# Kernel tuning notes

Hardware: AMD Instinct MI355X
Metric: run time of the kernel (lower is better)

## Reference

```python
import jax, jax.numpy as jnp
import numpy as np

N_CLS = 7  # only the first 7 channels contribute to the loss

def setup_inputs() -> dict:
    key = jax.random.key(0)
    k1, k2 = jax.random.split(key)
    pred = jax.random.normal(k1, (256, 16384, 8), dtype=jnp.float32)
    gt = jax.random.normal(k2, (256, 16384, 8), dtype=jnp.float32)
    return {"pred": pred, "gt": gt}

def reference(pred, gt):
    # per-batch loss: sum over objects and first 7 channels of squared error
    diff = pred[..., :N_CLS] - gt[..., :N_CLS]  # [B, N, 7]
    return jnp.sum(diff * diff, axis=(1, 2))    # [B]
```

## Files before the change

kernel.cpp:

```cpp
#include <hip/hip_runtime.h>


#define THREADS 256
#define SPLIT 16
#define F4_PER_BATCH (16384 * 2)
#define F4_PER_BLOCK (F4_PER_BATCH / SPLIT)
#define UNROLL 8

__global__ __launch_bounds__(THREADS) void label_loss_kernel(
    const float4* __restrict__ pred,
    const float4* __restrict__ gt,
    float* __restrict__ out)
{
    const int bx  = blockIdx.x;
    const int b   = bx / SPLIT;
    const int seg = bx % SPLIT;
    const long i0 = (long)b * F4_PER_BATCH + (long)seg * F4_PER_BLOCK
                  + threadIdx.x;

    const float m = (threadIdx.x & 1) ? 0.0f : 1.0f;

    float4 p[UNROLL], g[UNROLL];
    #pragma unroll
    for (int k = 0; k < UNROLL; ++k) p[k] = pred[i0 + k * THREADS];
    #pragma unroll
    for (int k = 0; k < UNROLL; ++k) g[k] = gt[i0 + k * THREADS];

    float acc[UNROLL];
    #pragma unroll
    for (int k = 0; k < UNROLL; ++k) {
        const float dx = p[k].x - g[k].x;
        const float dy = p[k].y - g[k].y;
        const float dz = p[k].z - g[k].z;
        const float dw = p[k].w - g[k].w;
        acc[k] = dx * dx + dy * dy + dz * dz + m * (dw * dw);
    }

    float v = ((acc[0] + acc[1]) + (acc[2] + acc[3]))
            + ((acc[4] + acc[5]) + (acc[6] + acc[7]));

    #pragma unroll
    for (int off = 32; off > 0; off >>= 1)
        v += __shfl_down(v, off, 64);

    __shared__ float wsum[THREADS / 64];
    const int lane = threadIdx.x & 63;
    const int wave = threadIdx.x >> 6;
    if (lane == 0) wsum[wave] = v;
    __syncthreads();

    if (threadIdx.x == 0) {
        atomicAdd(&out[b], wsum[0] + wsum[1] + wsum[2] + wsum[3]);
    }
}

extern "C" void kernel_launch(void* const* d_in, const int* in_sizes, int n_in,
                              void* d_out, int out_size, void* d_ws, size_t ws_size,
                              hipStream_t stream) {
    const float4* pred = (const float4*)d_in[0];
    const float4* gt   = (const float4*)d_in[1];
    float* out = (float*)d_out;

    hipMemsetAsync(d_out, 0, (size_t)out_size * sizeof(float), stream);

    const int n_blocks = 256 * SPLIT;
    label_loss_kernel<<<dim3(n_blocks), dim3(THREADS), 0, stream>>>(pred, gt, out);
}
```

Measured before the change: 271.9 us.

## Use fewer blocks with a double-buffered chunk loop per thread

The split per batch drops from 16 to 4 blocks. Each thread now walks 8 chunks of 4 float4 pairs, with register double buffering so the loads for the next chunk are issued before the current chunk is consumed. This is meant to cut block launch and atomic overhead and keep loads in flight across iterations. In exchange there are fewer blocks (1024) to spread across the GPU, which may reduce memory-level parallelism. Register use per thread also goes up.

```diff
diff --git a/kernel.cpp b/kernel.cpp
--- a/kernel.cpp
+++ b/kernel.cpp
@@ -2,42 +2,64 @@
 
 
 #define THREADS 256
-#define SPLIT 16
+#define SPLIT 4
 #define F4_PER_BATCH (16384 * 2)
 #define F4_PER_BLOCK (F4_PER_BATCH / SPLIT)
-#define UNROLL 8
+#define DEPTH 4
+#define CHUNK (THREADS * DEPTH)
+#define NCHUNK (F4_PER_BLOCK / CHUNK)
 
 __global__ __launch_bounds__(THREADS) void label_loss_kernel(
     const float4* __restrict__ pred,
     const float4* __restrict__ gt,
     float* __restrict__ out)
 {
-    const int bx  = blockIdx.x;
-    const int b   = bx / SPLIT;
-    const int seg = bx % SPLIT;
-    const long i0 = (long)b * F4_PER_BATCH + (long)seg * F4_PER_BLOCK
-                  + threadIdx.x;
+    const int b   = blockIdx.x / SPLIT;
+    const int seg = blockIdx.x % SPLIT;
+    const long base = (long)b * F4_PER_BATCH + (long)seg * F4_PER_BLOCK
+                    + threadIdx.x;
 
     const float m = (threadIdx.x & 1) ? 0.0f : 1.0f;
 
-    float4 p[UNROLL], g[UNROLL];
-    #pragma unroll
-    for (int k = 0; k < UNROLL; ++k) p[k] = pred[i0 + k * THREADS];
-    #pragma unroll
-    for (int k = 0; k < UNROLL; ++k) g[k] = gt[i0 + k * THREADS];
+    float4 Pa[DEPTH], Ga[DEPTH], Pb[DEPTH], Gb[DEPTH];
+    float acc[DEPTH] = {0.0f, 0.0f, 0.0f, 0.0f};
 
-    float acc[UNROLL];
-    #pragma unroll
-    for (int k = 0; k < UNROLL; ++k) {
-        const float dx = p[k].x - g[k].x;
-        const float dy = p[k].y - g[k].y;
-        const float dz = p[k].z - g[k].z;
-        const float dw = p[k].w - g[k].w;
-        acc[k] = dx * dx + dy * dy + dz * dz + m * (dw * dw);
+#define LOAD(P_, G_, c) do {                                          \
+    const long o_ = base + (long)(c) * CHUNK;                         \
+    _Pragma("unroll")                                                 \
+    for (int k = 0; k < DEPTH; ++k) P_[k] = pred[o_ + k * THREADS];   \
+    _Pragma("unroll")                                                 \
+    for (int k = 0; k < DEPTH; ++k) G_[k] = gt[o_ + k * THREADS];     \
+  } while (0)
+
+#define CONSUME(P_, G_) do {                                          \
+    _Pragma("unroll")                                                 \
+    for (int k = 0; k < DEPTH; ++k) {                                 \
+      const float dx = P_[k].x - G_[k].x;                             \
+      const float dy = P_[k].y - G_[k].y;                             \
+      const float dz = P_[k].z - G_[k].z;                             \
+      const float dw = P_[k].w - G_[k].w;                             \
+      acc[k] += dx * dx + dy * dy + dz * dz + m * (dw * dw);          \
+    }                                                                 \
+  } while (0)
+
+    LOAD(Pa, Ga, 0);
+
+    #pragma unroll 1
+    for (int c = 0; c + 2 < NCHUNK; c += 2) {
+        LOAD(Pb, Gb, c + 1);
+        CONSUME(Pa, Ga);
+        LOAD(Pa, Ga, c + 2);
+        CONSUME(Pb, Gb);
     }
+    LOAD(Pb, Gb, NCHUNK - 1);
+    CONSUME(Pa, Ga);
+    CONSUME(Pb, Gb);
 
-    float v = ((acc[0] + acc[1]) + (acc[2] + acc[3]))
-            + ((acc[4] + acc[5]) + (acc[6] + acc[7]));
+#undef LOAD
+#undef CONSUME
+
+    float v = (acc[0] + acc[1]) + (acc[2] + acc[3]);
 
     #pragma unroll
     for (int off = 32; off > 0; off >>= 1)
```

New measurement: 277.2 us. About the same (+1.9%).
